# Performance work log

Measured on AMD Instinct MI355X. Metric: run time of the kernel, lower is better.

## Reference

```python
import jax, jax.numpy as jnp
import numpy as np

B, L, D, H = 2, 2048, 1024, 16
HD = D // H

def setup_inputs() -> dict:
    key = jax.random.key(0)
    ks = jax.random.split(key, 9)
    s = 1.0 / np.sqrt(D)
    return {
        "x": jax.random.normal(ks[0], (B, L, D), jnp.float32),
        "Wq": jax.random.normal(ks[1], (D, D), jnp.float32) * s,
        "bq": jax.random.normal(ks[2], (D,), jnp.float32) * 0.02,
        "Wk": jax.random.normal(ks[3], (D, D), jnp.float32) * s,
        "bk": jax.random.normal(ks[4], (D,), jnp.float32) * 0.02,
        "Wv": jax.random.normal(ks[5], (D, D), jnp.float32) * s,
        "bv": jax.random.normal(ks[6], (D,), jnp.float32) * 0.02,
        "Wo": jax.random.normal(ks[7], (D, D), jnp.float32) * s,
        "bo": jax.random.normal(ks[8], (D,), jnp.float32) * 0.02,
    }

def reference(x, Wq, bq, Wk, bk, Wv, bv, Wo, bo):
    b, l, d = x.shape
    # projections -> [B, H, L, HD]
    def split_heads(t):
        return t.reshape(b, l, H, HD).transpose(0, 2, 1, 3)
    Q = split_heads(x @ Wq + bq)
    K = split_heads(x @ Wk + bk)
    V = split_heads(x @ Wv + bv)
    scores = jnp.einsum('bhqd,bhkd->bhqk', Q, K)  # [B,H,L,L]
    causal = jnp.tril(jnp.ones((l, l), bool))
    scores = jnp.where(causal, scores, -jnp.inf)
    attn = jax.nn.softmax(scores / np.sqrt(HD), axis=-1)
    ctx = jnp.einsum('bhqk,bhkd->bhqd', attn, V)
    ctx = ctx.transpose(0, 2, 1, 3).reshape(b, l, d)
    return ctx @ Wo + bo
```

## Files before the change

### kernel.cpp

```cpp
#include <hip/hip_runtime.h>
#include <stdint.h>

typedef unsigned short u16;
typedef __attribute__((ext_vector_type(8))) __bf16 bf16x8;
typedef __attribute__((ext_vector_type(4))) float f32x4;
typedef __attribute__((ext_vector_type(16))) float f32x16;

__device__ __forceinline__ u16 f2bf(float f) {
  union { float f; uint32_t u; } c; c.f = f;
  uint32_t u = c.u + 0x7fffu + ((c.u >> 16) & 1u);
  return (u16)(u >> 16);
}
__device__ __forceinline__ uint32_t cvtpk(float a, float b) {
  uint32_t r;
  asm("v_cvt_pk_bf16_f32 %0, %1, %2" : "=v"(r) : "v"(a), "v"(b));
  return r;
}

__device__ __forceinline__ void async16(const u16* g, u16* l) {
  __builtin_amdgcn_global_load_lds(
      (const __attribute__((address_space(1))) void*)g,
      (__attribute__((address_space(3))) void*)l, 16, 0, 0);
}

__device__ __forceinline__ f32x4 mfma16(bf16x8 a, bf16x8 b, f32x4 c) {
  return __builtin_amdgcn_mfma_f32_16x16x32_bf16(a, b, c, 0, 0, 0);
}
__device__ __forceinline__ f32x16 mfma32(bf16x8 a, bf16x8 b, f32x16 c) {
  return __builtin_amdgcn_mfma_f32_32x32x16_bf16(a, b, c, 0, 0, 0);
}


__global__ __launch_bounds__(256) void x_cvt_kernel(const float* __restrict__ x,
                                                    u16* __restrict__ xb) {
  int i = (blockIdx.x * 256 + threadIdx.x) * 4;
  float4 v = *(const float4*)(x + i);
  uint2 t; t.x = cvtpk(v.x, v.y); t.y = cvtpk(v.z, v.w);
  *(uint2*)(xb + i) = t;
}

__global__ __launch_bounds__(256) void wt_cvt_kernel(const float* __restrict__ Wq,
                                                     const float* __restrict__ Wk,
                                                     const float* __restrict__ Wv,
                                                     const float* __restrict__ Wo,
                                                     u16* __restrict__ out) {
  __shared__ __align__(16) u16 t[64][72];
  int z = blockIdx.z;
  const float* W = (z == 0) ? Wq : (z == 1) ? Wk : (z == 2) ? Wv : Wo;
  u16* o = out + (size_t)z * (1u << 20);
  int n0 = blockIdx.x * 64, k0 = blockIdx.y * 64;
  int tid = threadIdx.x;
  int c4 = (tid & 15) * 4, r0 = tid >> 4;
#pragma unroll
  for (int i = 0; i < 4; i++) {
    int r = r0 + i * 16;
    float4 v = *(const float4*)(W + (size_t)(k0 + r) * 1024 + n0 + c4);
    t[c4 + 0][r] = f2bf(v.x);
    t[c4 + 1][r] = f2bf(v.y);
    t[c4 + 2][r] = f2bf(v.z);
    t[c4 + 3][r] = f2bf(v.w);
  }
  __syncthreads();
  int n = tid >> 2, kc = (tid & 3) * 16;
  uint4 a = *(const uint4*)&t[n][kc];
  uint4 b = *(const uint4*)&t[n][kc + 8];
  *(uint4*)(o + (size_t)(n0 + n) * 1024 + k0 + kc) = a;
  *(uint4*)(o + (size_t)(n0 + n) * 1024 + k0 + kc + 8) = b;
}

template <int TN>
__device__ __forceinline__ void gemm_core2(const u16* __restrict__ A,
                                           const u16* __restrict__ Bt,
                                           u16* As, u16* Bs,
                                           f32x4 (&acc)[4][TN / 32]) {
  constexpr int NJ = TN / 32;
  constexpr int ASZ = 128 * 32, BSZ = TN * 32;
  const int tid = threadIdx.x, wave = tid >> 6, lane = tid & 63;
  const int low = lane & 15, hi = lane >> 4;
  const int wm = wave >> 1, wn = wave & 1;
  const int m0 = blockIdx.y * 128, n0 = blockIdx.x * TN;
  const f32x4 fzero = {0.f, 0.f, 0.f, 0.f};
#pragma unroll
  for (int i = 0; i < 4; i++)
#pragma unroll
    for (int j = 0; j < NJ; j++) acc[i][j] = fzero;

  const int ea0 = wave * 128 + lane, ea1 = ea0 + 64;
  const u16* ga0 = A + (size_t)(m0 + (ea0 >> 2)) * 1024 + (ea0 & 3) * 8;
  const u16* ga1 = A + (size_t)(m0 + (ea1 >> 2)) * 1024 + (ea1 & 3) * 8;
  u16* la0 = As + (wave * 2 + 0) * 512;
  u16* la1 = As + (wave * 2 + 1) * 512;

  const int eb0 = (TN == 128) ? (wave * 128 + lane) : (wave * 64 + lane);
  const int eb1 = eb0 + 64;
  const u16* gb0 = Bt + (size_t)(n0 + (eb0 >> 2)) * 1024 + (eb0 & 3) * 8;
  const u16* gb1 = Bt + (size_t)(n0 + (eb1 >> 2)) * 1024 + (eb1 & 3) * 8;
  u16* lb0 = Bs + ((TN == 128) ? (wave * 2 + 0) * 512 : wave * 512);
  u16* lb1 = Bs + (wave * 2 + 1) * 512;

  const u16* ap = As + (wm * 64 + low) * 32 + hi * 8;
  const u16* bp = Bs + (wn * (TN / 2) + low) * 32 + hi * 8;

#define GSTAGE(buf, KT)                                                        \
  {                                                                            \
    async16(ga0 + (KT), la0 + (buf) * ASZ);                                    \
    async16(ga1 + (KT), la1 + (buf) * ASZ);                                    \
    async16(gb0 + (KT), lb0 + (buf) * BSZ);                                    \
    if (TN == 128) async16(gb1 + (KT), lb1 + (buf) * BSZ);                     \
  }

  GSTAGE(0, 0)
  __syncthreads();
  int buf = 0;
  for (int kt = 0; kt < 1024; kt += 32) {
    if (kt + 32 < 1024) GSTAGE(buf ^ 1, kt + 32)
    bf16x8 af[4], bfv[NJ];
#pragma unroll
    for (int i = 0; i < 4; i++)
      af[i] = *(const bf16x8*)(ap + buf * ASZ + i * 16 * 32);
#pragma unroll
    for (int j = 0; j < NJ; j++)
      bfv[j] = *(const bf16x8*)(bp + buf * BSZ + j * 16 * 32);
#pragma unroll
    for (int i = 0; i < 4; i++)
#pragma unroll
      for (int j = 0; j < NJ; j++) acc[i][j] = mfma16(af[i], bfv[j], acc[i][j]);
    __syncthreads();
    buf ^= 1;
  }
#undef GSTAGE
}

__global__ __launch_bounds__(256) void gemm_qkv_kernel(
    const u16* __restrict__ xb, const u16* __restrict__ wT,
    const float* __restrict__ bq, const float* __restrict__ bk,
    const float* __restrict__ bv,
    u16* __restrict__ qs, u16* __restrict__ ks, u16* __restrict__ vts) {
  __shared__ __align__(16) u16 As[2 * 128 * 32];
  __shared__ __align__(16) u16 Bs[2 * 128 * 32];
  const int z = blockIdx.z;
  const u16* Bt = wT + (size_t)z * (1u << 20);
  f32x4 acc[4][4];
  gemm_core2<128>(xb, Bt, As, Bs, acc);

  const float* bias = (z == 0) ? bq : (z == 1) ? bk : bv;
  u16* out = (z == 0) ? qs : (z == 1) ? ks : vts;
  const float scale = (z == 0) ? 0.180336880f : 1.0f;
  const int tid = threadIdx.x, wave = tid >> 6, lane = tid & 63;
  const int low = lane & 15, hi = lane >> 4;
  const int wm = wave >> 1, wn = wave & 1;
  const int m0 = blockIdx.y * 128, n0 = blockIdx.x * 128;
#pragma unroll
  for (int i = 0; i < 4; i++)
#pragma unroll
    for (int j = 0; j < 4; j++) {
      int gn = n0 + wn * 64 + j * 16 + low;
      float bval = bias[gn];
      int h = gn >> 6, hd = gn & 63;
#pragma unroll
      for (int r = 0; r < 4; r++) {
        int gm = m0 + wm * 64 + i * 16 + hi * 4 + r;
        int b = gm >> 11, l = gm & 2047;
        float v = (acc[i][j][r] + bval) * scale;
        size_t addr;
        if (z == 2) {
          int lp = (l & ~12) | ((l & 4) << 1) | ((l & 8) >> 1);
          addr = ((size_t)((b * 16 + h) * 64 + hd)) * 2048 + lp;
        } else {
          addr = ((size_t)((b * 16 + h) * 2048 + l)) * 64 + hd;
        }
        out[addr] = f2bf(v);
      }
    }
}

__global__ __launch_bounds__(256) void gemm_out_kernel(
    const u16* __restrict__ ctx, const u16* __restrict__ woT,
    const float* __restrict__ bo, float* __restrict__ out) {
  __shared__ __align__(16) u16 As[2 * 128 * 32];
  __shared__ __align__(16) u16 Bs[2 * 64 * 32];
  f32x4 acc[4][2];
  gemm_core2<64>(ctx, woT, As, Bs, acc);
  const int tid = threadIdx.x, wave = tid >> 6, lane = tid & 63;
  const int low = lane & 15, hi = lane >> 4;
  const int wm = wave >> 1, wn = wave & 1;
  const int m0 = blockIdx.y * 128, n0 = blockIdx.x * 64;
#pragma unroll
  for (int i = 0; i < 4; i++)
#pragma unroll
    for (int j = 0; j < 2; j++) {
      int gn = n0 + wn * 32 + j * 16 + low;
      float bval = bo[gn];
#pragma unroll
      for (int r = 0; r < 4; r++) {
        int gm = m0 + wm * 64 + i * 16 + hi * 4 + r;
        out[(size_t)gm * 1024 + gn] = acc[i][j][r] + bval;
      }
    }
}

__global__ __launch_bounds__(256) void flash_kernel(
    const u16* __restrict__ Qs, const u16* __restrict__ Ks,
    const u16* __restrict__ Vts, u16* __restrict__ ctx) {
  __shared__ __align__(16) u16 Kls[3][64 * 64];
  __shared__ __align__(16) u16 Vls[3][64 * 64];

  const int bid = blockIdx.x;
  const int qt = (bid < 256) ? (15 - (bid >> 5)) : ((bid - 256) >> 5);
  const int bh = bid & 31;
  const int qb = qt * 128;
  const int nkv = 2 * qt + 2;

  const int tid = threadIdx.x, wave = tid >> 6, lane = tid & 63;
  const int q32 = lane & 31, hi2 = lane >> 5;
  const int x7 = q32 & 7;

  const u16* Qb = Qs + (size_t)bh * (2048 * 64);
  const u16* Kb = Ks + (size_t)bh * (2048 * 64);
  const u16* Vb = Vts + (size_t)bh * (64 * 2048);

  const int qrow = qb + wave * 32 + q32;
  bf16x8 qf[4];
#pragma unroll
  for (int ds = 0; ds < 4; ds++)
    qf[ds] = *(const bf16x8*)(Qb + (size_t)qrow * 64 + ds * 16 + hi2 * 8);

  f32x16 o0, o1;
#pragma unroll
  for (int r = 0; r < 16; r++) { o0[r] = 0.f; o1[r] = 0.f; }
  float m_ = -1e30f, l_ = 0.f;

  const int srow0 = (lane >> 3);
  const int scc = lane & 7;

#define STAGE(buf, KT0)                                                        \
  {                                                                            \
    _Pragma("unroll") for (int i = 0; i < 2; i++) {                            \
      int row = (wave * 2 + i) * 8 + srow0;                                    \
      async16(Kb + (size_t)((KT0) + row) * 64 + ((scc ^ (row & 7)) * 8),       \
              &Kls[buf][(wave * 2 + i) * 512]);                                \
      async16(Vb + (size_t)row * 2048 + (KT0) + ((scc ^ (row & 7)) * 8),       \
              &Vls[buf][(wave * 2 + i) * 512]);                                \
    }                                                                          \
  }

  STAGE(0, 0)
  STAGE(1, 64)

  const int qmax = qb + wave * 32 + 31;

  int c0 = 0, c1 = 1, c2 = 2;
  for (int t = 0; t < nkv; t++) {
    const int kt0 = t * 64;
    if (t + 1 < nkv) { asm volatile("s_waitcnt vmcnt(4)" ::: "memory"); }
    else             { asm volatile("s_waitcnt vmcnt(0)" ::: "memory"); }
    __builtin_amdgcn_s_barrier();
    if (t + 2 < nkv) STAGE(c2, kt0 + 128)

    if (kt0 <= qmax) {
      const u16* Kc = &Kls[c0][0];
      const u16* Vc = &Vls[c0][0];

      f32x16 s0, s1;
#pragma unroll
      for (int r = 0; r < 16; r++) { s0[r] = 0.f; s1[r] = 0.f; }
      __builtin_amdgcn_s_setprio(1);
#pragma unroll
      for (int ds = 0; ds < 4; ds++) {
        int cs = ((ds * 2 + hi2) ^ x7) * 8;
        bf16x8 kf0 = *(const bf16x8*)(Kc + q32 * 64 + cs);
        bf16x8 kf1 = *(const bf16x8*)(Kc + (32 + q32) * 64 + cs);
        s0 = mfma32(kf0, qf[ds], s0);
        s1 = mfma32(kf1, qf[ds], s1);
      }
      __builtin_amdgcn_s_setprio(0);

      bf16x8 vf0[4], vf1[4];
#pragma unroll
      for (int ksx = 0; ksx < 4; ksx++) {
        int sc = ((2 * ksx + hi2) ^ x7) * 8;
        vf0[ksx] = *(const bf16x8*)(Vc + q32 * 64 + sc);
        vf1[ksx] = *(const bf16x8*)(Vc + (32 + q32) * 64 + sc);
      }

      if (kt0 + 63 > qb + wave * 32) {
#pragma unroll
        for (int r = 0; r < 16; r++) {
          int kl = (r & 3) + 8 * (r >> 2) + 4 * hi2;
          if (kt0 + kl > qrow) s0[r] = -1e30f;
          if (kt0 + 32 + kl > qrow) s1[r] = -1e30f;
        }
      }

      float pm = -1e30f;
#pragma unroll
      for (int r = 0; r < 16; r++) pm = fmaxf(pm, fmaxf(s0[r], s1[r]));
      pm = fmaxf(pm, __shfl_xor(pm, 32));
      if (__any(pm > m_ + 8.f)) {
        float mn = fmaxf(m_, pm);
        float corr = __builtin_amdgcn_exp2f(m_ - mn);
        m_ = mn;
        l_ *= corr;
#pragma unroll
        for (int r = 0; r < 16; r++) { o0[r] *= corr; o1[r] *= corr; }
      }

      float rs = 0.f;
#pragma unroll
      for (int r = 0; r < 16; r++) {
        s0[r] = __builtin_amdgcn_exp2f(s0[r] - m_);
        s1[r] = __builtin_amdgcn_exp2f(s1[r] - m_);
        rs += s0[r] + s1[r];
      }
      rs += __shfl_xor(rs, 32);
      l_ += rs;

      bf16x8 pb[4];
#pragma unroll
      for (int ksx = 0; ksx < 4; ksx++) {
        union { uint32_t u[4]; bf16x8 v; } pu;
        if (ksx < 2) {
          int rb = 8 * ksx;
          pu.u[0] = cvtpk(s0[rb + 0], s0[rb + 1]);
          pu.u[1] = cvtpk(s0[rb + 2], s0[rb + 3]);
          pu.u[2] = cvtpk(s0[rb + 4], s0[rb + 5]);
          pu.u[3] = cvtpk(s0[rb + 6], s0[rb + 7]);
        } else {
          int rb = 8 * (ksx - 2);
          pu.u[0] = cvtpk(s1[rb + 0], s1[rb + 1]);
          pu.u[1] = cvtpk(s1[rb + 2], s1[rb + 3]);
          pu.u[2] = cvtpk(s1[rb + 4], s1[rb + 5]);
          pu.u[3] = cvtpk(s1[rb + 6], s1[rb + 7]);
        }
        pb[ksx] = pu.v;
      }

      __builtin_amdgcn_s_setprio(1);
#pragma unroll
      for (int ksx = 0; ksx < 4; ksx++) {
        o0 = mfma32(vf0[ksx], pb[ksx], o0);
        o1 = mfma32(vf1[ksx], pb[ksx], o1);
      }
      __builtin_amdgcn_s_setprio(0);
    }

    int tmp = c0; c0 = c1; c1 = c2; c2 = tmp;
  }

  const int b = bh >> 4, h = bh & 15;
  float inv = 1.f / l_;
  size_t base = ((size_t)(b * 2048 + qrow)) * 1024 + h * 64;
#pragma unroll
  for (int m = 0; m < 4; m++) {
    uint2 w0, w1;
    w0.x = cvtpk(o0[4 * m + 0] * inv, o0[4 * m + 1] * inv);
    w0.y = cvtpk(o0[4 * m + 2] * inv, o0[4 * m + 3] * inv);
    *(uint2*)(ctx + base + 8 * m + 4 * hi2) = w0;
    w1.x = cvtpk(o1[4 * m + 0] * inv, o1[4 * m + 1] * inv);
    w1.y = cvtpk(o1[4 * m + 2] * inv, o1[4 * m + 3] * inv);
    *(uint2*)(ctx + base + 32 + 8 * m + 4 * hi2) = w1;
  }
}


extern "C" void kernel_launch(void* const* d_in, const int* in_sizes, int n_in,
                              void* d_out, int out_size, void* d_ws, size_t ws_size,
                              hipStream_t stream) {
  const float* x  = (const float*)d_in[0];
  const float* Wq = (const float*)d_in[1];
  const float* bq = (const float*)d_in[2];
  const float* Wk = (const float*)d_in[3];
  const float* bk = (const float*)d_in[4];
  const float* Wv = (const float*)d_in[5];
  const float* bv = (const float*)d_in[6];
  const float* Wo = (const float*)d_in[7];
  const float* bo = (const float*)d_in[8];

  char* ws = (char*)d_ws;
  u16* xb  = (u16*)(ws);
  u16* wT  = (u16*)(ws + (8u << 20));
  u16* qs  = (u16*)(ws + (16u << 20));
  u16* ks  = (u16*)(ws + (24u << 20));
  u16* vts = (u16*)(ws + (32u << 20));
  u16* ctx = (u16*)(ws + (40u << 20));

  x_cvt_kernel<<<4096, 256, 0, stream>>>(x, xb);
  wt_cvt_kernel<<<dim3(16, 16, 4), 256, 0, stream>>>(Wq, Wk, Wv, Wo, wT);
  gemm_qkv_kernel<<<dim3(8, 32, 3), 256, 0, stream>>>(xb, wT, bq, bk, bv, qs, ks, vts);
  flash_kernel<<<512, 256, 0, stream>>>(qs, ks, vts, ctx);
  gemm_out_kernel<<<dim3(16, 32), 256, 0, stream>>>(ctx, wT + 3 * (1u << 20), bo, (float*)d_out);
}
```

Before: 132.3 us.

## Split flash attention KV range across two wave groups and merge partials

The flash kernel now launches 512 threads per block and splits the causal KV tiles into two halves, one for each group of four waves. Each group keeps its own triple-buffered K/V staging in LDS. At the end, group 1 writes its partial output, running max and sum into LDS, and group 0 rescales and combines them before the final write. This halves the serial KV loop length per query tile to cut latency on the long tiles. The cost is more waves per block, doubled LDS use, an extra merge step with two block barriers, and possibly lower occupancy.

```diff
diff --git a/kernel.cpp b/kernel.cpp
--- a/kernel.cpp
+++ b/kernel.cpp
@@ -199,19 +199,20 @@
     }
 }
 
-__global__ __launch_bounds__(256) void flash_kernel(
+__global__ __launch_bounds__(512) void flash_kernel(
     const u16* __restrict__ Qs, const u16* __restrict__ Ks,
     const u16* __restrict__ Vts, u16* __restrict__ ctx) {
-  __shared__ __align__(16) u16 Kls[3][64 * 64];
-  __shared__ __align__(16) u16 Vls[3][64 * 64];
+  __shared__ __align__(16) u16 Kls[2][3][64 * 64];
+  __shared__ __align__(16) u16 Vls[2][3][64 * 64];
 
   const int bid = blockIdx.x;
   const int qt = (bid < 256) ? (15 - (bid >> 5)) : ((bid - 256) >> 5);
   const int bh = bid & 31;
   const int qb = qt * 128;
-  const int nkv = 2 * qt + 2;
+  const int nT = qt + 1;
 
   const int tid = threadIdx.x, wave = tid >> 6, lane = tid & 63;
+  const int wq = wave & 3, g = wave >> 2;
   const int q32 = lane & 31, hi2 = lane >> 5;
   const int x7 = q32 & 7;
 
@@ -219,7 +220,7 @@
   const u16* Kb = Ks + (size_t)bh * (2048 * 64);
   const u16* Vb = Vts + (size_t)bh * (64 * 2048);
 
-  const int qrow = qb + wave * 32 + q32;
+  const int qrow = qb + wq * 32 + q32;
   bf16x8 qf[4];
 #pragma unroll
   for (int ds = 0; ds < 4; ds++)
@@ -229,37 +230,37 @@
 #pragma unroll
   for (int r = 0; r < 16; r++) { o0[r] = 0.f; o1[r] = 0.f; }
   float m_ = -1e30f, l_ = 0.f;
-
-  const int srow0 = (lane >> 3);
-  const int scc = lane & 7;
 
 #define STAGE(buf, KT0)                                                        \
   {                                                                            \
     _Pragma("unroll") for (int i = 0; i < 2; i++) {                            \
-      int row = (wave * 2 + i) * 8 + srow0;                                    \
-      async16(Kb + (size_t)((KT0) + row) * 64 + ((scc ^ (row & 7)) * 8),       \
-              &Kls[buf][(wave * 2 + i) * 512]);                                \
-      async16(Vb + (size_t)row * 2048 + (KT0) + ((scc ^ (row & 7)) * 8),       \
-              &Vls[buf][(wave * 2 + i) * 512]);                                \
+      int row = (wq * 2 + i) * 8 + (lane >> 3);                                \
+      async16(Kb + (size_t)((KT0) + row) * 64 +                                \
+                  (((lane & 7) ^ (row & 7)) * 8),                              \
+              &Kls[g][buf][(wq * 2 + i) * 512]);                               \
+      async16(Vb + (size_t)row * 2048 + (KT0) +                                \
+                  (((lane & 7) ^ (row & 7)) * 8),                              \
+              &Vls[g][buf][(wq * 2 + i) * 512]);                               \
     }                                                                          \
   }
 
-  STAGE(0, 0)
-  STAGE(1, 64)
-
-  const int qmax = qb + wave * 32 + 31;
+  const int tb = g * nT;
+  STAGE(0, (tb + 0) * 64)
+  STAGE(1, (tb + 1) * 64)
+
+  const int qmax = qb + wq * 32 + 31;
 
   int c0 = 0, c1 = 1, c2 = 2;
-  for (int t = 0; t < nkv; t++) {
-    const int kt0 = t * 64;
-    if (t + 1 < nkv) { asm volatile("s_waitcnt vmcnt(4)" ::: "memory"); }
-    else             { asm volatile("s_waitcnt vmcnt(0)" ::: "memory"); }
+  for (int t = 0; t < nT; t++) {
+    const int kt0 = (tb + t) * 64;
+    if (t + 1 < nT) { asm volatile("s_waitcnt vmcnt(4)" ::: "memory"); }
+    else            { asm volatile("s_waitcnt vmcnt(0)" ::: "memory"); }
     __builtin_amdgcn_s_barrier();
-    if (t + 2 < nkv) STAGE(c2, kt0 + 128)
+    if (t + 2 < nT) STAGE(c2, (tb + t + 2) * 64)
 
     if (kt0 <= qmax) {
-      const u16* Kc = &Kls[c0][0];
-      const u16* Vc = &Vls[c0][0];
+      const u16* Kc = &Kls[g][c0][0];
+      const u16* Vc = &Vls[g][c0][0];
 
       f32x16 s0, s1;
 #pragma unroll
@@ -283,7 +284,7 @@
         vf1[ksx] = *(const bf16x8*)(Vc + (32 + q32) * 64 + sc);
       }
 
-      if (kt0 + 63 > qb + wave * 32) {
+      if (kt0 + 63 > qb + wq * 32) {
 #pragma unroll
         for (int r = 0; r < 16; r++) {
           int kl = (r & 3) + 8 * (r >> 2) + 4 * hi2;
@@ -347,18 +348,51 @@
     int tmp = c0; c0 = c1; c1 = c2; c2 = tmp;
   }
 
-  const int b = bh >> 4, h = bh & 15;
-  float inv = 1.f / l_;
-  size_t base = ((size_t)(b * 2048 + qrow)) * 1024 + h * 64;
-#pragma unroll
-  for (int m = 0; m < 4; m++) {
-    uint2 w0, w1;
-    w0.x = cvtpk(o0[4 * m + 0] * inv, o0[4 * m + 1] * inv);
-    w0.y = cvtpk(o0[4 * m + 2] * inv, o0[4 * m + 3] * inv);
-    *(uint2*)(ctx + base + 8 * m + 4 * hi2) = w0;
-    w1.x = cvtpk(o1[4 * m + 0] * inv, o1[4 * m + 1] * inv);
-    w1.y = cvtpk(o1[4 * m + 2] * inv, o1[4 * m + 3] * inv);
-    *(uint2*)(ctx + base + 32 + 8 * m + 4 * hi2) = w1;
+  __syncthreads();
+  float* mb = (float*)&Kls[0][0][0] + wq * 2304;
+  if (g == 1) {
+#pragma unroll
+    for (int m = 0; m < 4; m++) {
+      f32x4 qa = {o0[4 * m + 0], o0[4 * m + 1], o0[4 * m + 2], o0[4 * m + 3]};
+      f32x4 qb2 = {o1[4 * m + 0], o1[4 * m + 1], o1[4 * m + 2], o1[4 * m + 3]};
+      *(f32x4*)(mb + m * 256 + (lane << 2)) = qa;
+      *(f32x4*)(mb + (4 + m) * 256 + (lane << 2)) = qb2;
+    }
+    mb[2048 + (lane << 1) + 0] = m_;
+    mb[2048 + (lane << 1) + 1] = l_;
+  }
+  __syncthreads();
+  if (g == 0) {
+    float m1 = mb[2048 + (lane << 1) + 0];
+    float l1 = mb[2048 + (lane << 1) + 1];
+    float mm = fmaxf(m_, m1);
+    float cA = __builtin_amdgcn_exp2f(m_ - mm);
+    float cB = __builtin_amdgcn_exp2f(m1 - mm);
+    l_ = l_ * cA + l1 * cB;
+#pragma unroll
+    for (int m = 0; m < 4; m++) {
+      f32x4 qa = *(const f32x4*)(mb + m * 256 + (lane << 2));
+      f32x4 qb2 = *(const f32x4*)(mb + (4 + m) * 256 + (lane << 2));
+#pragma unroll
+      for (int j = 0; j < 4; j++) {
+        o0[4 * m + j] = o0[4 * m + j] * cA + qa[j] * cB;
+        o1[4 * m + j] = o1[4 * m + j] * cA + qb2[j] * cB;
+      }
+    }
+
+    const int b = bh >> 4, h = bh & 15;
+    float inv = 1.f / l_;
+    size_t base = ((size_t)(b * 2048 + qrow)) * 1024 + h * 64;
+#pragma unroll
+    for (int m = 0; m < 4; m++) {
+      uint2 w0, w1;
+      w0.x = cvtpk(o0[4 * m + 0] * inv, o0[4 * m + 1] * inv);
+      w0.y = cvtpk(o0[4 * m + 2] * inv, o0[4 * m + 3] * inv);
+      *(uint2*)(ctx + base + 8 * m + 4 * hi2) = w0;
+      w1.x = cvtpk(o1[4 * m + 0] * inv, o1[4 * m + 1] * inv);
+      w1.y = cvtpk(o1[4 * m + 2] * inv, o1[4 * m + 3] * inv);
+      *(uint2*)(ctx + base + 32 + 8 * m + 4 * hi2) = w1;
+    }
   }
 }
 
@@ -387,6 +421,6 @@
   x_cvt_kernel<<<4096, 256, 0, stream>>>(x, xb);
   wt_cvt_kernel<<<dim3(16, 16, 4), 256, 0, stream>>>(Wq, Wk, Wv, Wo, wT);
   gemm_qkv_kernel<<<dim3(8, 32, 3), 256, 0, stream>>>(xb, wT, bq, bk, bv, qs, ks, vts);
-  flash_kernel<<<512, 256, 0, stream>>>(qs, ks, vts, ctx);
+  flash_kernel<<<512, 512, 0, stream>>>(qs, ks, vts, ctx);
   gemm_out_kernel<<<dim3(16, 32), 256, 0, stream>>>(ctx, wT + 3 * (1u << 20), bo, (float*)d_out);
 }
```

After: 124.6 us. 1.06x faster.
